# Kernel optimization log

Measured on AMD Instinct MI355X. Metric: run time of the kernel, lower is better.

The kernel has to match this reference:

```python
import jax, jax.numpy as jnp
import numpy as np

D_IN, D_H, BATCH = 4096, 512, 8192


def _layernorm(x, g, b, eps=1e-5):
    mu = jnp.mean(x, axis=-1, keepdims=True)
    var = jnp.var(x, axis=-1, keepdims=True)
    return (x - mu) * jax.lax.rsqrt(var + eps) * g + b


def setup_inputs() -> dict:
    key = jax.random.key(0)
    ks = jax.random.split(key, 10)
    x = jax.random.normal(ks[0], (BATCH, D_IN), jnp.float32)
    h = jax.random.normal(ks[1], (BATCH, D_H), jnp.float32)
    s1 = 1.0 / np.sqrt(D_IN + D_H)
    W1 = jax.random.uniform(ks[2], (D_IN + D_H, D_H), jnp.float32, -s1, s1)
    b1 = jnp.zeros((D_H,), jnp.float32)
    ln1_g = jnp.ones((D_H,), jnp.float32)
    ln1_b = jnp.zeros((D_H,), jnp.float32)
    s2 = 1.0 / np.sqrt(D_H)
    W2 = jax.random.uniform(ks[3], (D_H, 3 * D_H), jnp.float32, -s2, s2)
    b2 = jnp.zeros((3 * D_H,), jnp.float32)
    base_tau = jnp.ones((D_H,), jnp.float32)  # time_constant_init = 1.0
    base_A = jax.random.normal(ks[4], (D_H, D_H), jnp.float32) * 0.1
    idx = jnp.arange(D_H)
    base_A = base_A.at[idx, idx].set(-0.5)
    base_B = jax.random.normal(ks[5], (D_IN, D_H), jnp.float32) * 0.1
    hn_g = jnp.ones((D_H,), jnp.float32)
    hn_b = jnp.zeros((D_H,), jnp.float32)
    return {"x": x, "h": h, "W1": W1, "b1": b1, "ln1_g": ln1_g, "ln1_b": ln1_b,
            "W2": W2, "b2": b2, "base_tau": base_tau, "base_A": base_A,
            "base_B": base_B, "hn_g": hn_g, "hn_b": hn_b}


def reference(x, h, W1, b1, ln1_g, ln1_b, W2, b2, base_tau, base_A, base_B, hn_g, hn_b):
    dt = 0.1
    # time_net hypernetwork
    xh = jnp.concatenate([x, h], axis=-1)                 # [B, D_IN+D_H]
    t = _layernorm(xh @ W1 + b1, ln1_g, ln1_b)
    t = jax.nn.gelu(t, approximate=False)
    params = t @ W2 + b2                                  # [B, 3*D_H]
    tau_s, A_s, B_s = jnp.split(params, 3, axis=-1)
    tau = base_tau * (jax.nn.sigmoid(tau_s) * 2.0)        # [B, D_H]
    A_row = 1.0 + 0.5 * jnp.tanh(A_s)                     # per-sample row scale of A
    B_col = 1.0 + 0.5 * jnp.tanh(B_s)                     # per-sample col scale of B
    # A[b] = base_A * A_row[b][:,None]; h @ A[b].T == (h @ base_A.T) * A_row[b]
    recurrent = (h @ base_A.T) * A_row                    # [B, D_H]
    # B[b] = base_B * B_col[b][None,:]; x @ B[b] == (x @ base_B) * B_col[b]
    input_term = (x @ base_B) * B_col                     # [B, D_H]
    dhdt = -h / (tau + 1e-8) + jnp.tanh(recurrent + input_term)
    new_h = _layernorm(h + dt * dhdt, hn_g, hn_b)
    return new_h
```

## Files before the change

kernel.cpp:

```cpp
#include <hip/hip_runtime.h>

#define BATCH 8192
#define DIN 4096
#define DH 512

typedef float f32x4 __attribute__((ext_vector_type(4)));
typedef float f32x2 __attribute__((ext_vector_type(2)));
typedef short s16x8 __attribute__((ext_vector_type(8)));
typedef unsigned short u16x2 __attribute__((ext_vector_type(2)));
typedef unsigned short u16x4 __attribute__((ext_vector_type(4)));
typedef unsigned short u16x8 __attribute__((ext_vector_type(8)));

static __device__ __forceinline__ unsigned short f2bf(float f) {
  unsigned int u = __float_as_uint(f);
  u += 0x7FFFu + ((u >> 16) & 1u);
  return (unsigned short)(u >> 16);
}
static __device__ __forceinline__ float bf2f(unsigned short s) {
  return __uint_as_float(((unsigned int)s) << 16);
}

typedef const __attribute__((address_space(1))) unsigned int* gas_ptr;
typedef __attribute__((address_space(3))) unsigned int* las_ptr;
static __device__ __forceinline__ void gl_lds16(const unsigned short* g, unsigned short* l) {
  __builtin_amdgcn_global_load_lds((gas_ptr)g, (las_ptr)l, 16, 0, 0);
}

__global__ __launch_bounds__(256) void cast_bf16_k(
    const float* __restrict__ in, unsigned short* __restrict__ out)
{
  const int i = (blockIdx.x * 256 + threadIdx.x) * 4;
  f32x4 v = *(const f32x4*)(in + i);
  u16x4 p = { f2bf(v[0]), f2bf(v[1]), f2bf(v[2]), f2bf(v[3]) };
  *(u16x4*)(out + i) = p;
}

static __device__ __forceinline__ void transpose_body(
    const float* __restrict__ in, int C,
    unsigned short* __restrict__ out, int ldo, int row_off,
    int bx, int by, float (*tl)[33])
{
  const int tid = threadIdx.x;
  const int tx = tid & 31, ty = tid >> 5;
  const int c0 = bx * 32, r0 = by * 32;
#pragma unroll
  for (int i = 0; i < 4; i++)
    tl[ty + 8 * i][tx] = in[(size_t)(r0 + ty + 8 * i) * C + c0 + tx];
  __syncthreads();
#pragma unroll
  for (int i = 0; i < 4; i++)
    out[(size_t)(row_off + c0 + ty + 8 * i) * ldo + r0 + tx] = f2bf(tl[tx][ty + 8 * i]);
}

__global__ __launch_bounds__(256) void prep_small_k(
    const float* __restrict__ h, unsigned short* __restrict__ hbf,
    const float* __restrict__ base_A, unsigned short* __restrict__ Abf,
    const float* __restrict__ W1, const float* __restrict__ base_B,
    unsigned short* __restrict__ BTcat,
    const float* __restrict__ W2, unsigned short* __restrict__ W2T)
{
  __shared__ float tl[32][33];
  const int b = blockIdx.x;
  const int tid = threadIdx.x;
  const int KC = DIN + DH;
  if (b < 4096) {
    const int i = (b * 256 + tid) * 4;
    f32x4 v = *(const f32x4*)(h + i);
    u16x4 p = { f2bf(v[0]), f2bf(v[1]), f2bf(v[2]), f2bf(v[3]) };
    *(u16x4*)(hbf + i) = p;
  } else if (b < 4352) {
    const int i = ((b - 4096) * 256 + tid) * 4;
    f32x4 v = *(const f32x4*)(base_A + i);
    u16x4 p = { f2bf(v[0]), f2bf(v[1]), f2bf(v[2]), f2bf(v[3]) };
    *(u16x4*)(Abf + i) = p;
  } else if (b < 6656) {
    const int bb = b - 4352;
    transpose_body(W1, DH, BTcat, KC, 0, bb & 15, bb >> 4, tl);
  } else if (b < 8704) {
    const int bb = b - 6656;
    transpose_body(base_B, DH, BTcat, KC, DH, bb & 15, bb >> 4, tl);
  } else if (b < 8832) {
    const int gid = (b - 8704) * 256 + tid;
    const int row = gid >> 6, c = (gid & 63) * 8;
    u16x8 z = { 0, 0, 0, 0, 0, 0, 0, 0 };
    *(u16x8*)(BTcat + (size_t)(DH + row) * KC + DIN + c) = z;
  } else {
    const int bb = b - 8832;
    transpose_body(W2, 3 * DH, W2T, DH, 0, bb % 48, bb / 48, tl);
  }
}

template<int EPI, int DEPTH>
static __device__ __forceinline__ void gemm_engine(
    const unsigned short* __restrict__ A0, int lda0, int K0,
    const unsigned short* __restrict__ A1, int lda1,
    const unsigned short* __restrict__ BT, int ldb,
    unsigned short* __restrict__ C0, int ldc,
    unsigned short* __restrict__ C1,
    const float* __restrict__ bias,
    const float* __restrict__ base_tau,
    int mb, int nb, int K,
    unsigned short* As, unsigned short* Bs)
{
  const int tid = threadIdx.x;
  const int lane = tid & 63;
  const int wid = tid >> 6;
  const int wm = (wid >> 1) * 64;
  const int wn = (wid & 1) * 64;
  const int srow = lane >> 2;
  const int scol = (lane & 3) * 8;
  const int fr = lane & 15;
  const int fk = (lane >> 4) * 8;
  const int NT = K / 32;

  f32x4 acc[4][4];
#pragma unroll
  for (int i = 0; i < 4; i++)
#pragma unroll
    for (int j = 0; j < 4; j++)
      acc[i][j] = (f32x4){ 0.f, 0.f, 0.f, 0.f };

  auto STAGE = [&](int buf, int t) {
    const int k0 = t * 32;
    const bool s0 = (k0 < K0);
    const unsigned short* Ab = s0 ? A0 : A1;
    const int ld = s0 ? lda0 : lda1;
    const int ko = (s0 ? k0 : k0 - K0) + scol;
    unsigned short* ab = As + buf * 4096 + (32 * wid) * 32;
    unsigned short* bb = Bs + buf * 4096 + (32 * wid) * 32;
#pragma unroll
    for (int c = 0; c < 2; c++) {
      const int r = 32 * wid + c * 16 + srow;
      gl_lds16(Ab + (size_t)(mb + r) * ld + ko, ab + c * 16 * 32);
      gl_lds16(BT + (size_t)(nb + r) * ldb + k0 + scol, bb + c * 16 * 32);
    }
  };

#pragma unroll
  for (int d = 0; d < DEPTH - 1; d++) STAGE(d, d);
  if (DEPTH == 4) asm volatile("s_waitcnt vmcnt(8)" ::: "memory");
  else            asm volatile("s_waitcnt vmcnt(4)" ::: "memory");
  __builtin_amdgcn_s_barrier();

  for (int t = 0; t < NT; t++) {
    if (t + DEPTH - 1 < NT) STAGE((t + DEPTH - 1) % DEPTH, t + DEPTH - 1);

    const unsigned short* ar = As + (t % DEPTH) * 4096;
    const unsigned short* br = Bs + (t % DEPTH) * 4096;
    s16x8 af[4], bv[4];
#pragma unroll
    for (int mi = 0; mi < 4; mi++)
      af[mi] = *(const s16x8*)(ar + (wm + mi * 16 + fr) * 32 + fk);
#pragma unroll
    for (int ni = 0; ni < 4; ni++)
      bv[ni] = *(const s16x8*)(br + (wn + ni * 16 + fr) * 32 + fk);

    asm volatile("s_waitcnt lgkmcnt(0)" ::: "memory");
    __builtin_amdgcn_sched_barrier(0);

#pragma unroll
    for (int mi = 0; mi < 4; mi++)
#pragma unroll
      for (int ni = 0; ni < 4; ni++)
        acc[mi][ni] = __builtin_amdgcn_mfma_f32_16x16x32_bf16(
            af[mi], bv[ni], acc[mi][ni], 0, 0, 0);

    if (t + 1 < NT) {
      const int rem = NT - 2 - t;
      const int nw = (rem < DEPTH - 2) ? rem : DEPTH - 2;
      if (nw >= 2)      asm volatile("s_waitcnt vmcnt(8)" ::: "memory");
      else if (nw == 1) asm volatile("s_waitcnt vmcnt(4)" ::: "memory");
      else              asm volatile("s_waitcnt vmcnt(0)" ::: "memory");
      __builtin_amdgcn_s_barrier();
    }
  }

  const int rb = (lane >> 4) * 4;
#pragma unroll
  for (int mi = 0; mi < 4; mi++) {
#pragma unroll
    for (int ni = 0; ni < 4; ni++) {
#pragma unroll
      for (int r = 0; r < 4; r++) {
        const int row = mb + wm + mi * 16 + rb + r;
        const int col = nb + wn + ni * 16 + fr;
        float v = acc[mi][ni][r];
        if (EPI == 3) {
          if (col < DH) C0[(size_t)row * DH + col] = f2bf(v + bias[col]);
          else          C1[(size_t)row * DH + (col - DH)] = f2bf(v);
        } else if (EPI == 2) {
          C0[(size_t)row * ldc + col] = f2bf(v);
        } else if (EPI == 1) {
          v += bias[col];
          if ((col >> 9) == 0) {
            const float s = 1.0f / (1.0f + expf(-v));
            v = 1.0f / (base_tau[col & (DH - 1)] * 2.0f * s + 1e-8f);
          } else {
            v = 1.0f + 0.5f * tanhf(v);
          }
          C0[(size_t)row * ldc + col] = f2bf(v);
        }
      }
    }
  }
}

__global__ __launch_bounds__(256) void fused_gemm_k(
    const unsigned short* __restrict__ xbf,
    const unsigned short* __restrict__ hbf,
    const unsigned short* __restrict__ BTcat,
    unsigned short* __restrict__ pre1,
    unsigned short* __restrict__ rawB,
    const float* __restrict__ b1)
{
  __shared__ unsigned short As[4 * 4096];
  __shared__ unsigned short Bs[4 * 4096];
  const int cpx = gridDim.x >> 3;
  const int virt = (blockIdx.x & 7) * cpx + (blockIdx.x >> 3);
  const int mb = (virt & 63) * 128;
  const int nb = (virt >> 6) * 128;
  gemm_engine<3, 4>(xbf, DIN, DIN, hbf, DH, BTcat, DIN + DH,
                    pre1, DH, rawB, b1, nullptr, mb, nb, DIN + DH, As, Bs);
}

__global__ __launch_bounds__(256) void tail_gemm_k(
    const unsigned short* __restrict__ hbf,
    const unsigned short* __restrict__ Abf,
    const unsigned short* __restrict__ tbf,
    const unsigned short* __restrict__ W2T,
    unsigned short* __restrict__ rawA,
    unsigned short* __restrict__ scales,
    const float* __restrict__ b2,
    const float* __restrict__ base_tau)
{
  __shared__ unsigned short As[3 * 4096];
  __shared__ unsigned short Bs[3 * 4096];
  const int b = blockIdx.x;
  if (b < 768) {
    const int mb = (b & 63) * 128, nb = (b >> 6) * 128;
    gemm_engine<1, 3>(tbf, DH, DH, nullptr, 0, W2T, DH,
                      scales, 3 * DH, nullptr, b2, base_tau, mb, nb, DH, As, Bs);
  } else {
    const int b2i = b - 768;
    const int mb = (b2i & 63) * 128, nb = (b2i >> 6) * 128;
    gemm_engine<2, 3>(hbf, DH, DH, nullptr, 0, Abf, DH,
                      rawA, DH, nullptr, nullptr, nullptr, mb, nb, DH, As, Bs);
  }
}

__device__ __forceinline__ float block_sum256(float v, float* red) {
#pragma unroll
  for (int m = 32; m >= 1; m >>= 1) v += __shfl_xor(v, m, 64);
  __syncthreads();
  if ((threadIdx.x & 63) == 0) red[threadIdx.x >> 6] = v;
  __syncthreads();
  return red[0] + red[1] + red[2] + red[3];
}

__global__ __launch_bounds__(256) void ln_gelu_k(
    const unsigned short* __restrict__ pre,
    const float* __restrict__ g, const float* __restrict__ b,
    unsigned short* __restrict__ t)
{
  __shared__ float red[4];
  const int row = blockIdx.x;
  const int c = threadIdx.x * 2;
  const size_t ro = (size_t)row * DH;
  u16x2 raw = *(const u16x2*)(pre + ro + c);
  const float v0 = bf2f(raw[0]), v1 = bf2f(raw[1]);
  const float mu = block_sum256(v0 + v1, red) * (1.0f / DH);
  const float d0 = v0 - mu, d1 = v1 - mu;
  const float var = block_sum256(d0 * d0 + d1 * d1, red) * (1.0f / DH);
  const float inv = rsqrtf(var + 1e-5f);
  const float y0 = d0 * inv * g[c] + b[c];
  const float y1 = d1 * inv * g[c + 1] + b[c + 1];
  u16x2 o = { f2bf(0.5f * y0 * (1.0f + erff(y0 * 0.70710678118f))),
              f2bf(0.5f * y1 * (1.0f + erff(y1 * 0.70710678118f))) };
  *(u16x2*)(t + ro + c) = o;
}

__global__ __launch_bounds__(256) void final_k(
    const float* __restrict__ h,
    const unsigned short* __restrict__ rawA,
    const unsigned short* __restrict__ rawB,
    const unsigned short* __restrict__ scales,
    const float* __restrict__ hn_g, const float* __restrict__ hn_b,
    float* __restrict__ out)
{
  __shared__ float red[4];
  const int row = blockIdx.x;
  const int c = threadIdx.x * 2;
  const size_t ro = (size_t)row * DH;
  f32x2 hv = *(const f32x2*)(h + ro + c);
  u16x2 ra = *(const u16x2*)(rawA + ro + c);
  u16x2 rb = *(const u16x2*)(rawB + ro + c);
  const unsigned short* sc = scales + (size_t)row * (3 * DH);
  u16x2 ti  = *(const u16x2*)(sc + c);
  u16x2 arw = *(const u16x2*)(sc + DH + c);
  u16x2 bcl = *(const u16x2*)(sc + 2 * DH + c);
  const float u0 = hv[0] + 0.1f * (-hv[0] * bf2f(ti[0])
                 + tanhf(bf2f(ra[0]) * bf2f(arw[0]) + bf2f(rb[0]) * bf2f(bcl[0])));
  const float u1 = hv[1] + 0.1f * (-hv[1] * bf2f(ti[1])
                 + tanhf(bf2f(ra[1]) * bf2f(arw[1]) + bf2f(rb[1]) * bf2f(bcl[1])));
  const float mu = block_sum256(u0 + u1, red) * (1.0f / DH);
  const float d0 = u0 - mu, d1 = u1 - mu;
  const float var = block_sum256(d0 * d0 + d1 * d1, red) * (1.0f / DH);
  const float inv = rsqrtf(var + 1e-5f);
  f32x2 o = { d0 * inv * hn_g[c] + hn_b[c],
              d1 * inv * hn_g[c + 1] + hn_b[c + 1] };
  *(f32x2*)(out + ro + c) = o;
}

extern "C" void kernel_launch(void* const* d_in, const int* in_sizes, int n_in,
                              void* d_out, int out_size, void* d_ws, size_t ws_size,
                              hipStream_t stream)
{
  const float* x        = (const float*)d_in[0];
  const float* h        = (const float*)d_in[1];
  const float* W1       = (const float*)d_in[2];
  const float* b1       = (const float*)d_in[3];
  const float* ln1_g    = (const float*)d_in[4];
  const float* ln1_b    = (const float*)d_in[5];
  const float* W2       = (const float*)d_in[6];
  const float* b2       = (const float*)d_in[7];
  const float* base_tau = (const float*)d_in[8];
  const float* base_A   = (const float*)d_in[9];
  const float* base_B   = (const float*)d_in[10];
  const float* hn_g     = (const float*)d_in[11];
  const float* hn_b     = (const float*)d_in[12];

  char* w = (char*)d_ws;
  unsigned short* xbf    = (unsigned short*)(w);
  unsigned short* hbf    = (unsigned short*)(w + 67108864);
  unsigned short* BTcat  = (unsigned short*)(w + 75497472);
  unsigned short* tbf    = (unsigned short*)(w + 75497472);
  unsigned short* W2T    = (unsigned short*)(w + 84934656);
  unsigned short* Abf    = (unsigned short*)(w + 86507520);
  unsigned short* pre1   = (unsigned short*)(w + 87031808);
  unsigned short* rawA   = (unsigned short*)(w + 87031808);
  unsigned short* rawB   = (unsigned short*)(w + 95420416);
  unsigned short* scales = (unsigned short*)(w + 103809024);

  cast_bf16_k<<<DIN * BATCH / 1024, 256, 0, stream>>>(x, xbf);
  prep_small_k<<<9600, 256, 0, stream>>>(h, hbf, base_A, Abf, W1, base_B, BTcat, W2, W2T);

  fused_gemm_k<<<512, 256, 0, stream>>>(xbf, hbf, BTcat, pre1, rawB, b1);
  ln_gelu_k<<<BATCH, 256, 0, stream>>>(pre1, ln1_g, ln1_b, tbf);
  tail_gemm_k<<<1024, 256, 0, stream>>>(hbf, Abf, tbf, W2T, rawA, scales, b2, base_tau);
  final_k<<<BATCH, 256, 0, stream>>>(h, rawA, rawB, scales, hn_g, hn_b, (float*)d_out);
}
```

Before: 236.3 us.

## Split GEMM K-loop across two wave groups with LDS reduction and swizzle

```diff
diff --git a/kernel.cpp b/kernel.cpp
--- a/kernel.cpp
+++ b/kernel.cpp
@@ -90,8 +90,8 @@
   }
 }
 
-template<int EPI, int DEPTH>
-static __device__ __forceinline__ void gemm_engine(
+template<int EPI>
+static __device__ __forceinline__ void gemm2_engine(
     const unsigned short* __restrict__ A0, int lda0, int K0,
     const unsigned short* __restrict__ A1, int lda1,
     const unsigned short* __restrict__ BT, int ldb,
@@ -99,19 +99,24 @@
     unsigned short* __restrict__ C1,
     const float* __restrict__ bias,
     const float* __restrict__ base_tau,
-    int mb, int nb, int K,
-    unsigned short* As, unsigned short* Bs)
-{
+    int mb, int nb, int K, char* smem)
+{
+  unsigned short* As = (unsigned short*)smem;
+  unsigned short* Bs = (unsigned short*)(smem + 32768);
+  float* red = (float*)smem;
+
   const int tid = threadIdx.x;
   const int lane = tid & 63;
   const int wid = tid >> 6;
-  const int wm = (wid >> 1) * 64;
-  const int wn = (wid & 1) * 64;
+  const int grp = wid >> 2;
+  const int wg  = wid & 3;
+  const int wm = (wg >> 1) * 64;
+  const int wn = (wg & 1) * 64;
   const int srow = lane >> 2;
-  const int scol = (lane & 3) * 8;
+  const int scol = ((lane & 3) ^ ((lane >> 3) & 3)) * 8;
   const int fr = lane & 15;
-  const int fk = (lane >> 4) * 8;
-  const int NT = K / 32;
+  const int fk = ((lane >> 4) ^ ((lane >> 1) & 3)) * 8;
+  const int NT2 = K / 64;
 
   f32x4 acc[4][4];
 #pragma unroll
@@ -120,33 +125,33 @@
     for (int j = 0; j < 4; j++)
       acc[i][j] = (f32x4){ 0.f, 0.f, 0.f, 0.f };
 
-  auto STAGE = [&](int buf, int t) {
-    const int k0 = t * 32;
+  auto STAGE = [&](int buf, int per) {
+    const int tk = 2 * per + grp;
+    const int k0 = tk * 32;
     const bool s0 = (k0 < K0);
     const unsigned short* Ab = s0 ? A0 : A1;
     const int ld = s0 ? lda0 : lda1;
     const int ko = (s0 ? k0 : k0 - K0) + scol;
-    unsigned short* ab = As + buf * 4096 + (32 * wid) * 32;
-    unsigned short* bb = Bs + buf * 4096 + (32 * wid) * 32;
+    unsigned short* ab = As + (grp * 2 + buf) * 4096 + (32 * wg) * 32;
+    unsigned short* bb = Bs + (grp * 2 + buf) * 4096 + (32 * wg) * 32;
 #pragma unroll
     for (int c = 0; c < 2; c++) {
-      const int r = 32 * wid + c * 16 + srow;
+      const int r = 32 * wg + c * 16 + srow;
       gl_lds16(Ab + (size_t)(mb + r) * ld + ko, ab + c * 16 * 32);
       gl_lds16(BT + (size_t)(nb + r) * ldb + k0 + scol, bb + c * 16 * 32);
     }
   };
 
-#pragma unroll
-  for (int d = 0; d < DEPTH - 1; d++) STAGE(d, d);
-  if (DEPTH == 4) asm volatile("s_waitcnt vmcnt(8)" ::: "memory");
-  else            asm volatile("s_waitcnt vmcnt(4)" ::: "memory");
+  STAGE(0, 0);
+  asm volatile("s_waitcnt vmcnt(0)" ::: "memory");
   __builtin_amdgcn_s_barrier();
 
-  for (int t = 0; t < NT; t++) {
-    if (t + DEPTH - 1 < NT) STAGE((t + DEPTH - 1) % DEPTH, t + DEPTH - 1);
-
-    const unsigned short* ar = As + (t % DEPTH) * 4096;
-    const unsigned short* br = Bs + (t % DEPTH) * 4096;
+  int buf = 0;
+  for (int t = 0; t < NT2; t++) {
+    if (t + 1 < NT2) STAGE(buf ^ 1, t + 1);
+
+    const unsigned short* ar = As + (grp * 2 + buf) * 4096;
+    const unsigned short* br = Bs + (grp * 2 + buf) * 4096;
     s16x8 af[4], bv[4];
 #pragma unroll
     for (int mi = 0; mi < 4; mi++)
@@ -165,21 +170,28 @@
         acc[mi][ni] = __builtin_amdgcn_mfma_f32_16x16x32_bf16(
             af[mi], bv[ni], acc[mi][ni], 0, 0, 0);
 
-    if (t + 1 < NT) {
-      const int rem = NT - 2 - t;
-      const int nw = (rem < DEPTH - 2) ? rem : DEPTH - 2;
-      if (nw >= 2)      asm volatile("s_waitcnt vmcnt(8)" ::: "memory");
-      else if (nw == 1) asm volatile("s_waitcnt vmcnt(4)" ::: "memory");
-      else              asm volatile("s_waitcnt vmcnt(0)" ::: "memory");
-      __builtin_amdgcn_s_barrier();
-    }
-  }
+    asm volatile("s_waitcnt vmcnt(0)" ::: "memory");
+    __builtin_amdgcn_s_barrier();
+    buf ^= 1;
+  }
+
+  if (grp == 1) {
+#pragma unroll
+    for (int mi = 0; mi < 4; mi++)
+#pragma unroll
+      for (int ni = 0; ni < 4; ni++)
+        *(f32x4*)(red + (((wg * 4 + mi) * 4 + ni) * 64 + lane) * 4) = acc[mi][ni];
+  }
+  __syncthreads();
+  if (grp != 0) return;
 
   const int rb = (lane >> 4) * 4;
 #pragma unroll
   for (int mi = 0; mi < 4; mi++) {
 #pragma unroll
     for (int ni = 0; ni < 4; ni++) {
+      f32x4 o = *(const f32x4*)(red + (((wg * 4 + mi) * 4 + ni) * 64 + lane) * 4);
+      acc[mi][ni] += o;
 #pragma unroll
       for (int r = 0; r < 4; r++) {
         const int row = mb + wm + mi * 16 + rb + r;
@@ -205,7 +217,7 @@
   }
 }
 
-__global__ __launch_bounds__(256) void fused_gemm_k(
+__global__ __launch_bounds__(512, 4) void fused_gemm_k(
     const unsigned short* __restrict__ xbf,
     const unsigned short* __restrict__ hbf,
     const unsigned short* __restrict__ BTcat,
@@ -213,17 +225,16 @@
     unsigned short* __restrict__ rawB,
     const float* __restrict__ b1)
 {
-  __shared__ unsigned short As[4 * 4096];
-  __shared__ unsigned short Bs[4 * 4096];
+  __shared__ __align__(16) char smem[65536];
   const int cpx = gridDim.x >> 3;
   const int virt = (blockIdx.x & 7) * cpx + (blockIdx.x >> 3);
   const int mb = (virt & 63) * 128;
   const int nb = (virt >> 6) * 128;
-  gemm_engine<3, 4>(xbf, DIN, DIN, hbf, DH, BTcat, DIN + DH,
-                    pre1, DH, rawB, b1, nullptr, mb, nb, DIN + DH, As, Bs);
-}
-
-__global__ __launch_bounds__(256) void tail_gemm_k(
+  gemm2_engine<3>(xbf, DIN, DIN, hbf, DH, BTcat, DIN + DH,
+                  pre1, DH, rawB, b1, nullptr, mb, nb, DIN + DH, smem);
+}
+
+__global__ __launch_bounds__(512, 4) void tail_gemm_k(
     const unsigned short* __restrict__ hbf,
     const unsigned short* __restrict__ Abf,
     const unsigned short* __restrict__ tbf,
@@ -233,18 +244,17 @@
     const float* __restrict__ b2,
     const float* __restrict__ base_tau)
 {
-  __shared__ unsigned short As[3 * 4096];
-  __shared__ unsigned short Bs[3 * 4096];
+  __shared__ __align__(16) char smem[65536];
   const int b = blockIdx.x;
   if (b < 768) {
     const int mb = (b & 63) * 128, nb = (b >> 6) * 128;
-    gemm_engine<1, 3>(tbf, DH, DH, nullptr, 0, W2T, DH,
-                      scales, 3 * DH, nullptr, b2, base_tau, mb, nb, DH, As, Bs);
+    gemm2_engine<1>(tbf, DH, DH, nullptr, 0, W2T, DH,
+                    scales, 3 * DH, nullptr, b2, base_tau, mb, nb, DH, smem);
   } else {
     const int b2i = b - 768;
     const int mb = (b2i & 63) * 128, nb = (b2i >> 6) * 128;
-    gemm_engine<2, 3>(hbf, DH, DH, nullptr, 0, Abf, DH,
-                      rawA, DH, nullptr, nullptr, nullptr, mb, nb, DH, As, Bs);
+    gemm2_engine<2>(hbf, DH, DH, nullptr, 0, Abf, DH,
+                    rawA, DH, nullptr, nullptr, nullptr, mb, nb, DH, smem);
   }
 }
 
@@ -344,8 +354,8 @@
   cast_bf16_k<<<DIN * BATCH / 1024, 256, 0, stream>>>(x, xbf);
   prep_small_k<<<9600, 256, 0, stream>>>(h, hbf, base_A, Abf, W1, base_B, BTcat, W2, W2T);
 
-  fused_gemm_k<<<512, 256, 0, stream>>>(xbf, hbf, BTcat, pre1, rawB, b1);
+  fused_gemm_k<<<512, 512, 0, stream>>>(xbf, hbf, BTcat, pre1, rawB, b1);
   ln_gelu_k<<<BATCH, 256, 0, stream>>>(pre1, ln1_g, ln1_b, tbf);
-  tail_gemm_k<<<1024, 256, 0, stream>>>(hbf, Abf, tbf, W2T, rawA, scales, b2, base_tau);
+  tail_gemm_k<<<1024, 512, 0, stream>>>(hbf, Abf, tbf, W2T, rawA, scales, b2, base_tau);
   final_k<<<BATCH, 256, 0, stream>>>(h, rawA, rawB, scales, hn_g, hn_b, (float*)d_out);
 }
```

After: 219.6 us. 1.08x faster.
